# Kernel tuning notes

Hardware: AMD Instinct MI355X
Metric: run time of the kernel (lower is better)

Reference implementation:

```python
import jax, jax.numpy as jnp
import numpy as np

N_QUAT = 4
VERONESE_DIM = 10
OUT_FEATURES = 132

# static index sets matching torch.triu_indices(4, 4)
_rows, _cols = np.triu_indices(N_QUAT)          # 10 upper-tri entries
_mask = _rows != _cols
TRIU_ROWS = jnp.asarray(_rows)
TRIU_COLS = jnp.asarray(_cols)
SYM_ROWS = jnp.asarray(_cols[_mask])            # mirrored lower-tri
SYM_COLS = jnp.asarray(_rows[_mask])
SYM_Z_IDX = jnp.asarray(np.nonzero(_mask)[0])


def setup_inputs() -> dict:
    key = jax.random.key(0)
    k_z, k_w1, k_w2 = jax.random.split(key, 3)
    B, D_IN, D_HID, D_OUT_NN = 65536, 256, 1024, 128
    z = jax.random.normal(k_z, (B, D_IN), dtype=jnp.float32)
    W1 = jax.random.normal(k_w1, (D_IN, D_HID), dtype=jnp.float32) * 0.02
    b1 = jnp.zeros((D_HID,), dtype=jnp.float32)
    W2 = jax.random.normal(k_w2, (D_HID, D_OUT_NN), dtype=jnp.float32) * 0.02
    b2 = jnp.zeros((D_OUT_NN,), dtype=jnp.float32)
    return {"z": z, "W1": W1, "b1": b1, "W2": W2, "b2": b2}


def _recover_quat(z_v):
    # z_v: (B, 10) -> symmetric (B, 4, 4) -> top eigenvector -> (B, 4)
    B = z_v.shape[0]
    M = jnp.zeros((B, N_QUAT, N_QUAT), dtype=z_v.dtype)
    M = M.at[:, TRIU_ROWS, TRIU_COLS].set(z_v)
    M = M.at[:, SYM_ROWS, SYM_COLS].set(z_v[:, SYM_Z_IDX])
    _, vecs = jnp.linalg.eigh(M)          # eigenvalues ascending
    q = vecs[:, :, -1]                    # eigenvector of largest eigenvalue
    sign = jnp.sign(q[:, 0:1] + 1e-9)
    return q * sign


def reference(z, W1, b1, W2, b2):
    orig_shape = z.shape
    zf = z.reshape(-1, orig_shape[-1])           # (B, in_features)
    q_pred = _recover_quat(zf[:, :VERONESE_DIM])  # (B, 4)
    h = jax.nn.relu(zf @ W1 + b1)
    others = h @ W2 + b2                          # (B, 128)
    B = zf.shape[0]
    out = jnp.zeros((B, OUT_FEATURES), dtype=zf.dtype)
    out = out.at[:, :N_QUAT].set(q_pred)          # quat_indices = [0,1,2,3]
    out = out.at[:, N_QUAT:].set(others)          # non_quat = [4..131]
    return out.reshape(*orig_shape[:-1], OUT_FEATURES)
```

## Files before the change

### kernel.cpp

```cpp
#include <hip/hip_runtime.h>


typedef short s16x8 __attribute__((ext_vector_type(8)));
typedef float f32x4 __attribute__((ext_vector_type(4)));
typedef float f32x16 __attribute__((ext_vector_type(16)));
typedef unsigned char u8;

__device__ __forceinline__ f32x16 mfma32(s16x8 a, s16x8 b, f32x16 c) {
    return __builtin_amdgcn_mfma_f32_32x32x16_bf16(a, b, c, 0, 0, 0);
}

__device__ __forceinline__ short f2bf(float f) {
    unsigned int u = __float_as_uint(f);
    u = (u + 0x7fffu + ((u >> 16) & 1u)) >> 16;
    return (short)u;
}

__device__ __forceinline__ unsigned cvt_pk(float lo, float hi) {
    unsigned r;
    asm("v_cvt_pk_bf16_f32 %0, %1, %2" : "=v"(r) : "v"(lo), "v"(hi));
    return r;
}

__device__ __forceinline__ void pl32swap(unsigned& a, unsigned& b) {
    asm("v_permlane32_swap_b32 %0, %1" : "+v"(a), "+v"(b));
}

__device__ __forceinline__ void gload_lds16(const void* g, void* l) {
    __builtin_amdgcn_global_load_lds(
        (const __attribute__((address_space(1))) unsigned int*)g,
        (__attribute__((address_space(3))) unsigned int*)l, 16, 0, 0);
}

__global__ __launch_bounds__(256) void prep_weights(
    const float* __restrict__ W1, const float* __restrict__ W2,
    uint4* __restrict__ w1t, uint4* __restrict__ w2t)
{
    int tid = blockIdx.x * 256 + threadIdx.x;
    int hl = (tid >> 5) & 1, r32 = tid & 31;
    union { short b[8]; uint4 v; } pk;
    if (tid < 32768) {
        int s  = (tid >> 6) & 15;
        int ct = (tid >> 10) & 1;
        int c  = tid >> 11;
        int k0 = s * 16 + hl * 8;
        int n1 = c * 64 + ct * 32 + r32;
        #pragma unroll
        for (int j = 0; j < 8; ++j)
            pk.b[j] = f2bf(W1[(k0 + j) * 1024 + n1]);
        w1t[tid] = pk.v;
    } else {
        int g  = tid - 32768;
        int nt = (g >> 6) & 3;
        int K  = g >> 8;
        int k0 = K * 16 + hl * 8;
        int n2 = nt * 32 + r32;
        #pragma unroll
        for (int j = 0; j < 8; ++j)
            pk.b[j] = f2bf(W2[(k0 + j) * 128 + n2]);
        w2t[g] = pk.v;
    }
}

__global__ __launch_bounds__(256, 2) void fused_all(
    const float* __restrict__ z, const float* __restrict__ b1,
    const float* __restrict__ b2, const uint4* __restrict__ w1t,
    const uint4* __restrict__ w2t, float* __restrict__ out)
{
    __shared__ __align__(16) u8 lds[69632];

    const int t    = threadIdx.x;
    const int lane = t & 63;
    const int w    = t >> 6;
    const int hl   = lane >> 5;
    const int r32  = lane & 31;
    const int bm0  = blockIdx.x * 128;
    const int rowbase = bm0 + w * 32;

    #pragma unroll
    for (int i = 0; i < 8; ++i) {
        int f = i * 256 + t;
        gload_lds16(w1t + f, lds + f * 16);
    }
    gload_lds16(b1 + t * 4, lds + 65536 + t * 16);

    if (lane < 32) {
        int row = rowbase + lane;
        const float* zr = z + (size_t)row * 256;
        float4 v0 = *(const float4*)(zr);
        float4 v1 = *(const float4*)(zr + 4);
        float2 v2 = *(const float2*)(zr + 8);

        float A[4][4] = {{v0.x, v0.y, v0.z, v0.w},
                         {v0.y, v1.x, v1.y, v1.z},
                         {v0.z, v1.y, v1.w, v2.x},
                         {v0.w, v1.z, v2.x, v2.y}};
        float V[4][4] = {{1.f, 0.f, 0.f, 0.f},
                         {0.f, 1.f, 0.f, 0.f},
                         {0.f, 0.f, 1.f, 0.f},
                         {0.f, 0.f, 0.f, 1.f}};

#define ROT(p, qq) do {                                                   \
        float apq  = A[p][qq];                                            \
        float tau  = (A[qq][qq] - A[p][p]) *                              \
                     __builtin_amdgcn_rcpf(2.0f * apq);                   \
        float tt   = __builtin_amdgcn_rcpf(                               \
                        fabsf(tau) +                                      \
                        __builtin_amdgcn_sqrtf(fmaf(tau, tau, 1.0f)));    \
        tt = copysignf(tt, tau);                                          \
        tt = (fabsf(apq) > 1e-20f) ? tt : 0.0f;                           \
        float cth = __builtin_amdgcn_rsqf(fmaf(tt, tt, 1.0f));            \
        float sth = tt * cth;                                             \
        _Pragma("unroll")                                                 \
        for (int k = 0; k < 4; ++k) {                                     \
            float akp = A[k][p], akq = A[k][qq];                          \
            A[k][p]  = cth * akp - sth * akq;                             \
            A[k][qq] = sth * akp + cth * akq;                             \
        }                                                                 \
        _Pragma("unroll")                                                 \
        for (int k = 0; k < 4; ++k) {                                     \
            float apk = A[p][k], aqk = A[qq][k];                          \
            A[p][k]  = cth * apk - sth * aqk;                             \
            A[qq][k] = sth * apk + cth * aqk;                             \
        }                                                                 \
        _Pragma("unroll")                                                 \
        for (int k = 0; k < 4; ++k) {                                     \
            float vkp = V[k][p], vkq = V[k][qq];                          \
            V[k][p]  = cth * vkp - sth * vkq;                             \
            V[k][qq] = sth * vkp + cth * vkq;                             \
        }                                                                 \
    } while (0)

        #pragma unroll 1
        for (int sweep = 0; sweep < 6; ++sweep) {
            ROT(0, 1); ROT(0, 2); ROT(0, 3); ROT(1, 2); ROT(1, 3); ROT(2, 3);
        }
#undef ROT

        float bv = A[0][0];
        float q0 = V[0][0], q1 = V[1][0], q2 = V[2][0], q3 = V[3][0];
        #pragma unroll
        for (int k = 1; k < 4; ++k) {
            bool better = A[k][k] > bv;
            bv = better ? A[k][k] : bv;
            q0 = better ? V[0][k] : q0;
            q1 = better ? V[1][k] : q1;
            q2 = better ? V[2][k] : q2;
            q3 = better ? V[3][k] : q3;
        }
        float sgn = (q0 + 1e-9f) >= 0.0f ? 1.0f : -1.0f;
        *(float4*)(out + (size_t)row * 132) =
            make_float4(sgn * q0, sgn * q1, sgn * q2, sgn * q3);
    }

    s16x8 zf[16];
    {
        const float* zp = z + (size_t)(rowbase + r32) * 256 + hl * 8;
        #pragma unroll
        for (int s = 0; s < 16; ++s) {
            float4 a0 = *(const float4*)(zp + s * 16);
            float4 a1 = *(const float4*)(zp + s * 16 + 4);
            union { unsigned u[4]; s16x8 v; } pk;
            pk.u[0] = cvt_pk(a0.x, a0.y);
            pk.u[1] = cvt_pk(a0.z, a0.w);
            pk.u[2] = cvt_pk(a1.x, a1.y);
            pk.u[3] = cvt_pk(a1.z, a1.w);
            zf[s] = pk.v;
        }
    }

    const f32x16 zero16 = {0.f,0.f,0.f,0.f, 0.f,0.f,0.f,0.f,
                           0.f,0.f,0.f,0.f, 0.f,0.f,0.f,0.f};
    f32x16 acc2[4];
    #pragma unroll
    for (int nt = 0; nt < 4; ++nt) acc2[nt] = zero16;

    __syncthreads();

    const u8* const aW0  = lds + lane * 16;
    const u8* const aW1  = lds + 32768 + lane * 16;
    const u8* const blsp = lds + 65536 + hl * 16;
    const s16x8* const w2b = (const s16x8*)w2t + lane;

    u8* const s1b0 = lds;
    u8* const s1b1 = lds + 32768;

    auto pack = [&](const f32x16& d, const u8* bb, int ct, s16x8* hfo) {
        unsigned Plo[4], Phi[4];
        #pragma unroll
        for (int g = 0; g < 4; ++g) {
            f32x4 bv = *(const f32x4*)(bb + ct * 128 + g * 32);
            Plo[g] = cvt_pk(fmaxf(d[4*g+0] + bv[0], 0.f),
                            fmaxf(d[4*g+1] + bv[1], 0.f));
            Phi[g] = cvt_pk(fmaxf(d[4*g+2] + bv[2], 0.f),
                            fmaxf(d[4*g+3] + bv[3], 0.f));
        }
        #pragma unroll
        for (int f = 0; f < 2; ++f) {
            unsigned a0 = Plo[2*f], b0 = Plo[2*f+1];
            unsigned a1 = Phi[2*f], b1_ = Phi[2*f+1];
            pl32swap(a0, b0);
            pl32swap(a1, b1_);
            union { unsigned u[4]; s16x8 v; } fr;
            fr.u[0] = a0; fr.u[1] = a1; fr.u[2] = b0; fr.u[3] = b1_;
            hfo[f] = fr.v;
        }
    };

    auto chunk = [&](int c, const u8* a, u8* s1dst, bool FIRST, bool LAST) {
        if (!FIRST) {
            asm volatile("s_waitcnt vmcnt(16)" ::: "memory");
        }
        __builtin_amdgcn_s_barrier();

        if (!LAST) {
            const uint4* s1 = w1t + (c + 1) * 2048;
            #pragma unroll
            for (int i = 0; i < 8; ++i) {
                int f = i * 256 + t;
                gload_lds16(s1 + f, s1dst + f * 16);
            }
        }

        const s16x8* w2c = w2b + c * 1024;
        s16x8 w2f[4][4];
        #pragma unroll
        for (int ks = 0; ks < 4; ++ks)
            #pragma unroll
            for (int nt = 0; nt < 4; ++nt)
                w2f[ks][nt] = w2c[(ks * 4 + nt) * 64];

        const u8* bb = blsp + c * 256;
        s16x8 hf[4];

        __builtin_amdgcn_s_setprio(1);
        f32x16 d0 = zero16, d1 = zero16;
        #pragma unroll
        for (int s = 0; s < 16; ++s) {
            s16x8 a0 = *(const s16x8*)(a + s * 1024);
            s16x8 a1 = *(const s16x8*)(a + (16 + s) * 1024);
            d0 = mfma32(a0, zf[s], d0);
            d1 = mfma32(a1, zf[s], d1);
        }
        __builtin_amdgcn_s_setprio(0);

        pack(d0, bb, 0, hf);
        pack(d1, bb, 1, hf + 2);

        __builtin_amdgcn_s_setprio(1);
        #pragma unroll
        for (int ks = 0; ks < 4; ++ks)
            #pragma unroll
            for (int nt = 0; nt < 4; ++nt)
                acc2[nt] = mfma32(hf[ks], w2f[ks][nt], acc2[nt]);
        __builtin_amdgcn_s_setprio(0);
    };

    chunk(0, aW0, s1b1, true, false);
    #pragma unroll 1
    for (int cc = 0; cc < 7; ++cc) {
        chunk(2 * cc + 1, aW1, s1b0, false, false);
        chunk(2 * cc + 2, aW0, s1b1, false, false);
    }
    chunk(15, aW1, s1b0, false, true);

    #pragma unroll
    for (int nt = 0; nt < 4; ++nt) {
        const float b2v = b2[nt * 32 + r32];
        #pragma unroll
        for (int r = 0; r < 16; ++r) {
            int m = (r & 3) + 8 * (r >> 2) + 4 * hl;
            out[(size_t)(bm0 + w * 32 + m) * 132 + 4 + nt * 32 + r32] =
                acc2[nt][r] + b2v;
        }
    }
}

extern "C" void kernel_launch(void* const* d_in, const int* in_sizes, int n_in,
                              void* d_out, int out_size, void* d_ws, size_t ws_size,
                              hipStream_t stream) {
    const float* z  = (const float*)d_in[0];
    const float* W1 = (const float*)d_in[1];
    const float* b1 = (const float*)d_in[2];
    const float* W2 = (const float*)d_in[3];
    const float* b2 = (const float*)d_in[4];
    float* out = (float*)d_out;

    uint4* w1t = (uint4*)d_ws;
    uint4* w2t = (uint4*)((char*)d_ws + 512 * 1024);

    hipLaunchKernelGGL(prep_weights, dim3(192), dim3(256), 0, stream,
                       W1, W2, w1t, w2t);
    hipLaunchKernelGGL(fused_all, dim3(512), dim3(256), 0, stream,
                       z, b1, b2, (const uint4*)w1t, (const uint4*)w2t, out);
}
```

Measured before the change: 75.01 us.

## Use 512-thread blocks with double-buffered two-chunk W1 staging per barrier

Blocks grow to 8 waves covering 256 rows, and the grid halves to 256 blocks. Each block now stages two W1 chunks (64KB) per group in a 132KB LDS double buffer. A group prefetches the next two chunks, computes both, then syncs, so the block pays half as many barriers and each W1 chunk is shared by twice as many rows. In exchange, occupancy drops to one block per CU, 256 blocks may not fill all CUs evenly, and the prefetch no longer uses an explicit vmcnt wait, relying on __syncthreads instead.

New measurement: 72.90 us. 1.03x faster.

```diff
diff --git a/kernel.cpp b/kernel.cpp
--- a/kernel.cpp
+++ b/kernel.cpp
@@ -62,27 +62,27 @@
     }
 }
 
-__global__ __launch_bounds__(256, 2) void fused_all(
+__global__ __launch_bounds__(512, 1) void fused_all(
     const float* __restrict__ z, const float* __restrict__ b1,
     const float* __restrict__ b2, const uint4* __restrict__ w1t,
     const uint4* __restrict__ w2t, float* __restrict__ out)
 {
-    __shared__ __align__(16) u8 lds[69632];
+    __shared__ __align__(16) u8 lds[135168];
 
     const int t    = threadIdx.x;
     const int lane = t & 63;
     const int w    = t >> 6;
     const int hl   = lane >> 5;
     const int r32  = lane & 31;
-    const int bm0  = blockIdx.x * 128;
+    const int bm0  = blockIdx.x * 256;
     const int rowbase = bm0 + w * 32;
 
     #pragma unroll
     for (int i = 0; i < 8; ++i) {
-        int f = i * 256 + t;
+        int f = i * 512 + t;
         gload_lds16(w1t + f, lds + f * 16);
     }
-    gload_lds16(b1 + t * 4, lds + 65536 + t * 16);
+    if (t < 256) gload_lds16(b1 + t * 4, lds + 131072 + t * 16);
 
     if (lane < 32) {
         int row = rowbase + lane;
@@ -177,13 +177,14 @@
 
     __syncthreads();
 
-    const u8* const aW0  = lds + lane * 16;
-    const u8* const aW1  = lds + 32768 + lane * 16;
-    const u8* const blsp = lds + 65536 + hl * 16;
+    const u8* const aA0 = lds +          lane * 16;
+    const u8* const aA1 = lds + 32768  + lane * 16;
+    const u8* const aB0 = lds + 65536  + lane * 16;
+    const u8* const aB1 = lds + 98304  + lane * 16;
+    u8* const sA = lds;
+    u8* const sB = lds + 65536;
+    const u8* const blsp = lds + 131072 + hl * 16;
     const s16x8* const w2b = (const s16x8*)w2t + lane;
-
-    u8* const s1b0 = lds;
-    u8* const s1b1 = lds + 32768;
 
     auto pack = [&](const f32x16& d, const u8* bb, int ct, s16x8* hfo) {
         unsigned Plo[4], Phi[4];
@@ -207,21 +208,7 @@
         }
     };
 
-    auto chunk = [&](int c, const u8* a, u8* s1dst, bool FIRST, bool LAST) {
-        if (!FIRST) {
-            asm volatile("s_waitcnt vmcnt(16)" ::: "memory");
-        }
-        __builtin_amdgcn_s_barrier();
-
-        if (!LAST) {
-            const uint4* s1 = w1t + (c + 1) * 2048;
-            #pragma unroll
-            for (int i = 0; i < 8; ++i) {
-                int f = i * 256 + t;
-                gload_lds16(s1 + f, s1dst + f * 16);
-            }
-        }
-
+    auto body = [&](int c, const u8* a) {
         const s16x8* w2c = w2b + c * 1024;
         s16x8 w2f[4][4];
         #pragma unroll
@@ -256,13 +243,25 @@
         __builtin_amdgcn_s_setprio(0);
     };
 
-    chunk(0, aW0, s1b1, true, false);
+    auto group = [&](int g, const u8* a0, const u8* a1, u8* dst, bool LASTG) {
+        if (!LASTG) {
+            const uint4* s1 = w1t + (2 * g + 2) * 2048;
+            #pragma unroll
+            for (int i = 0; i < 8; ++i) {
+                int f = i * 512 + t;
+                gload_lds16(s1 + f, dst + f * 16);
+            }
+        }
+        body(2 * g,     a0);
+        body(2 * g + 1, a1);
+        __syncthreads();
+    };
+
     #pragma unroll 1
-    for (int cc = 0; cc < 7; ++cc) {
-        chunk(2 * cc + 1, aW1, s1b0, false, false);
-        chunk(2 * cc + 2, aW0, s1b1, false, false);
-    }
-    chunk(15, aW1, s1b0, false, true);
+    for (int gg = 0; gg < 4; ++gg) {
+        group(2 * gg,     aA0, aA1, sB, false);
+        group(2 * gg + 1, aB0, aB1, sA, gg == 3);
+    }
 
     #pragma unroll
     for (int nt = 0; nt < 4; ++nt) {
@@ -270,7 +269,7 @@
         #pragma unroll
         for (int r = 0; r < 16; ++r) {
             int m = (r & 3) + 8 * (r >> 2) + 4 * hl;
-            out[(size_t)(bm0 + w * 32 + m) * 132 + 4 + nt * 32 + r32] =
+            out[(size_t)(rowbase + m) * 132 + 4 + nt * 32 + r32] =
                 acc2[nt][r] + b2v;
         }
     }
@@ -291,6 +290,6 @@
 
     hipLaunchKernelGGL(prep_weights, dim3(192), dim3(256), 0, stream,
                        W1, W2, w1t, w2t);
-    hipLaunchKernelGGL(fused_all, dim3(512), dim3(256), 0, stream,
+    hipLaunchKernelGGL(fused_all, dim3(256), dim3(512), 0, stream,
                        z, b1, b2, (const uint4*)w1t, (const uint4*)w2t, out);
 }
```
